# Performance work log

Measured on AMD Instinct MI355X. Metric: run time of the kernel, lower is better.

Reference implementation:

```python
import jax, jax.numpy as jnp
import numpy as np
from jax import lax

DIM = 512
HEADS = 8
SR = 2  # kernel_and_stride for the KV downsampling conv


def setup_inputs() -> dict:
    key = jax.random.key(0)
    k0, k1, k2, k3 = jax.random.split(key, 4)
    B, C, H, W = 4, DIM, 64, 64
    x = jax.random.normal(k0, (B, C, H, W), dtype=jnp.float32)
    # Conv weights in OIHW layout (matching torch)
    wq = jax.random.normal(k1, (C, C, 1, 1), dtype=jnp.float32) / np.sqrt(C)
    wkv = jax.random.normal(k2, (2 * C, C, SR, SR), dtype=jnp.float32) / np.sqrt(C * SR * SR)
    wout = jax.random.normal(k3, (C, C, 1, 1), dtype=jnp.float32) / np.sqrt(C)
    return {"x": x, "wq": wq, "wkv": wkv, "wout": wout}


def _attend(x, wq, wkv, wout):
    B, C, H, W = x.shape
    d = C // HEADS
    scale = d ** -0.5
    # to_q: 1x1 conv == channel matmul
    q = jnp.einsum('bchw,oc->bohw', x, wq[:, :, 0, 0])
    # to_kv: strided conv, downsamples spatial grid by SR
    kv = lax.conv_general_dilated(
        x, wkv, window_strides=(SR, SR), padding='VALID',
        dimension_numbers=('NCHW', 'OIHW', 'NCHW'))
    k, v = jnp.split(kv, 2, axis=1)  # each [B, C, H/SR, W/SR]

    def to_bhl(t):  # [B, (h d), X, Y] -> [B, h, X*Y, d]
        b, c, xh, xw = t.shape
        return t.reshape(b, HEADS, d, xh * xw).transpose(0, 1, 3, 2)

    qh, kh, vh = to_bhl(q), to_bhl(k), to_bhl(v)
    sim = jnp.einsum('bhid,bhjd->bhij', qh, kh) * scale
    attn = jax.nn.softmax(sim, axis=-1)
    out = jnp.einsum('bhij,bhjd->bhid', attn, vh)  # [B, h, HW, d]
    out = out.transpose(0, 1, 3, 2).reshape(B, C, H, W)
    return jnp.einsum('bchw,oc->bohw', out, wout[:, :, 0, 0])


def reference(x, wq, wkv, wout):
    return _attend(x, wq, wkv, wout)
```

## Files before the change

### kernel.cpp

```cpp
#include <hip/hip_runtime.h>
#include <hip/hip_bf16.h>

typedef __bf16 bf16x8 __attribute__((ext_vector_type(8)));
typedef float f32x4 __attribute__((ext_vector_type(4)));
typedef unsigned short ushort_t;
typedef ushort_t ushort8 __attribute__((ext_vector_type(8)));
typedef unsigned uint2v __attribute__((ext_vector_type(2)));
typedef unsigned uint4v __attribute__((ext_vector_type(4)));

#define DIM 512
#define HEADS 8
#define HD 64
#define HWN 4096
#define KVN 1024
#define KKV 2048
#define LOG2E 1.44269504f

__device__ __forceinline__ ushort_t f2bf(float f) {
    union { float f; unsigned u; } v; v.f = f;
    unsigned r = v.u + 0x7fffu + ((v.u >> 16) & 1u);
    return (ushort_t)(r >> 16);
}

__device__ __forceinline__ unsigned cvtpk(float lo, float hi) {
    unsigned r;
    asm("v_cvt_pk_bf16_f32 %0, %1, %2" : "=v"(r) : "v"(lo), "v"(hi));
    return r;
}

__device__ __forceinline__ void pl32swap(unsigned &a, unsigned &b) {
    asm("v_permlane32_swap_b32 %0, %1" : "+v"(a), "+v"(b));
}
__device__ __forceinline__ void pl16swap(unsigned &a, unsigned &b) {
    asm("v_permlane16_swap_b32 %0, %1" : "+v"(a), "+v"(b));
}

__device__ __forceinline__ bf16x8 frag4(unsigned a, unsigned b, unsigned c, unsigned d) {
    uint4v t; t[0] = a; t[1] = b; t[2] = c; t[3] = d;
    return __builtin_bit_cast(bf16x8, t);
}

__device__ __forceinline__ void gload_lds16(const ushort_t* g, ushort_t* l) {
    __builtin_amdgcn_global_load_lds(
        (const __attribute__((address_space(1))) unsigned int*)(const void*)g,
        (__attribute__((address_space(3))) unsigned int*)(void*)l,
        16, 0, 0);
}

__device__ __forceinline__ void drain_sync() {
    asm volatile("s_waitcnt vmcnt(0)" ::: "memory");
    __syncthreads();
}

__global__ __launch_bounds__(256) void cvt_w2_kernel(
        const float* __restrict__ wq, const float* __restrict__ wout,
        ushort_t* __restrict__ wqb, ushort_t* __restrict__ woutb) {
    int i = blockIdx.x * 256 + threadIdx.x;
    const float* src;
    ushort_t* dst;
    if (i < 32768) { src = &wq[(size_t)i * 8];              dst = &wqb[(size_t)i * 8]; }
    else           { src = &wout[(size_t)(i - 32768) * 8];  dst = &woutb[(size_t)(i - 32768) * 8]; }
    f32x4 v0 = *(const f32x4*)&src[0];
    f32x4 v1 = *(const f32x4*)&src[4];
    ushort8 w;
    w[0] = f2bf(v0[0]); w[1] = f2bf(v0[1]); w[2] = f2bf(v0[2]); w[3] = f2bf(v0[3]);
    w[4] = f2bf(v1[0]); w[5] = f2bf(v1[1]); w[6] = f2bf(v1[2]); w[7] = f2bf(v1[3]);
    *(ushort8*)dst = w;
}

__global__ __launch_bounds__(256) void cvt_xT_kernel(
        const float* __restrict__ x, ushort_t* __restrict__ xT) {
    const int b  = blockIdx.z;
    const int c0 = blockIdx.y * 64;
    const int p0 = blockIdx.x * 64;
    __shared__ ushort_t tile[64 * 72];

    const int tid = threadIdx.x;
    {
        int r = tid >> 2, pc = (tid & 3) * 16;
        const float* src = &x[((size_t)b * DIM + c0 + r) * HWN + p0 + pc];
        f32x4 v0 = *(const f32x4*)&src[0];
        f32x4 v1 = *(const f32x4*)&src[4];
        f32x4 v2 = *(const f32x4*)&src[8];
        f32x4 v3 = *(const f32x4*)&src[12];
        ushort8 w0, w1;
        w0[0]=f2bf(v0[0]); w0[1]=f2bf(v0[1]); w0[2]=f2bf(v0[2]); w0[3]=f2bf(v0[3]);
        w0[4]=f2bf(v1[0]); w0[5]=f2bf(v1[1]); w0[6]=f2bf(v1[2]); w0[7]=f2bf(v1[3]);
        w1[0]=f2bf(v2[0]); w1[1]=f2bf(v2[1]); w1[2]=f2bf(v2[2]); w1[3]=f2bf(v2[3]);
        w1[4]=f2bf(v3[0]); w1[5]=f2bf(v3[1]); w1[6]=f2bf(v3[2]); w1[7]=f2bf(v3[3]);
        *(ushort8*)&tile[r * 72 + pc]     = w0;
        *(ushort8*)&tile[r * 72 + pc + 8] = w1;
    }
    __syncthreads();
    {
        int p = tid >> 2, cc = (tid & 3) * 16;
        ushort8 w0, w1;
        #pragma unroll
        for (int j = 0; j < 8; ++j) {
            w0[j] = tile[(cc + j) * 72 + p];
            w1[j] = tile[(cc + 8 + j) * 72 + p];
        }
        ushort_t* dst = &xT[((size_t)b * HWN + p0 + p) * DIM + c0 + cc];
        *(ushort8*)&dst[0] = w0;
        *(ushort8*)&dst[8] = w1;
    }
}

__global__ __launch_bounds__(256) void cvt_wkvT_kernel(
        const float* __restrict__ wkv, ushort_t* __restrict__ wkvT) {
    int i = blockIdx.x * 256 + threadIdx.x;
    if (i >= 1024 * 512) return;
    int o2 = i >> 9, c = i & 511;
    f32x4 v = *(const f32x4*)&wkv[(size_t)i * 4];
    #pragma unroll
    for (int q = 0; q < 4; ++q)
        wkvT[(size_t)o2 * KKV + q * 512 + c] = f2bf(v[q]);
}

__device__ __forceinline__ void gemm_compute_512(
        const ushort_t* __restrict__ sA, const ushort_t* __restrict__ sB,
        int wm, int wn, int l15, int quad, f32x4 (&acc)[4][2]) {
    bf16x8 a[2][4], bb[2][2];
    #pragma unroll
    for (int kk = 0; kk < 2; ++kk) {
        #pragma unroll
        for (int i = 0; i < 4; ++i) {
            int ra = wm + i * 16 + l15;
            a[kk][i] = *(const bf16x8*)&sA[ra * 64 + (((kk * 4 + quad) ^ (ra & 7)) * 8)];
        }
        #pragma unroll
        for (int j = 0; j < 2; ++j) {
            int rb = wn + j * 16 + l15;
            bb[kk][j] = *(const bf16x8*)&sB[rb * 64 + (((kk * 4 + quad) ^ (rb & 7)) * 8)];
        }
    }
    #pragma unroll
    for (int i = 0; i < 4; ++i)
        #pragma unroll
        for (int j = 0; j < 2; ++j) {
            acc[i][j] = __builtin_amdgcn_mfma_f32_16x16x32_bf16(a[0][i], bb[0][j], acc[i][j], 0, 0, 0);
            acc[i][j] = __builtin_amdgcn_mfma_f32_16x16x32_bf16(a[1][i], bb[1][j], acc[i][j], 0, 0, 0);
        }
}

__global__ __launch_bounds__(512, 4) void qproj_kernel(
        const ushort_t* __restrict__ xT, const ushort_t* __restrict__ wqb,
        ushort_t* __restrict__ qs) {
    const int b  = blockIdx.z;
    const int m0 = blockIdx.y * 128;
    const int n0 = blockIdx.x * 128;

    __shared__ ushort_t shA[2][128 * 64];
    __shared__ ushort_t shB[2][128 * 64];

    const int tid  = threadIdx.x;
    const int wave = tid >> 6;
    const int lane = tid & 63;
    const int l15  = lane & 15;
    const int quad = lane >> 4;
    const int wm   = (wave >> 2) * 64;
    const int wn   = (wave & 3) * 32;
    const int r8   = lane >> 3;
    const int c8   = (lane & 7) ^ r8;

    const ushort_t* aS[2];
    const ushort_t* bS[2];
    #pragma unroll
    for (int g = 0; g < 2; ++g) {
        int row = g * 64 + wave * 8 + r8;
        aS[g] = &wqb[(size_t)(m0 + row) * DIM + c8 * 8];
        bS[g] = &xT[((size_t)b * HWN + n0 + row) * DIM + c8 * 8];
    }
    const int ldso = wave * 8 * 64;

    f32x4 zero = {0.f, 0.f, 0.f, 0.f};
    f32x4 acc[4][2];
    #pragma unroll
    for (int i = 0; i < 4; ++i)
        #pragma unroll
        for (int j = 0; j < 2; ++j) acc[i][j] = zero;

    #pragma unroll
    for (int g = 0; g < 2; ++g) {
        gload_lds16(aS[g], &shA[0][g * 4096 + ldso]);
        gload_lds16(bS[g], &shB[0][g * 4096 + ldso]);
    }
    drain_sync();

    for (int t = 0; t < 8; ++t) {
        const int cur = t & 1;
        if (t < 7) {
            const int ko = (t + 1) * 64;
            #pragma unroll
            for (int g = 0; g < 2; ++g) {
                gload_lds16(aS[g] + ko, &shA[cur ^ 1][g * 4096 + ldso]);
                gload_lds16(bS[g] + ko, &shB[cur ^ 1][g * 4096 + ldso]);
            }
        }
        gemm_compute_512(shA[cur], shB[cur], wm, wn, l15, quad, acc);
        drain_sync();
    }

    #pragma unroll
    for (int i = 0; i < 4; ++i)
        #pragma unroll
        for (int j = 0; j < 2; ++j)
            #pragma unroll
            for (int r = 0; r < 4; ++r) {
                int m = m0 + wm + i * 16 + quad * 4 + r;
                int n = n0 + wn + j * 16 + l15;
                qs[((size_t)b * DIM + m) * HWN + n] =
                    f2bf(acc[i][j][r] * (0.125f * LOG2E));
            }
}

__global__ __launch_bounds__(512, 4) void kv_kernel(
        const ushort_t* __restrict__ xT, const ushort_t* __restrict__ wkvT,
        ushort_t* __restrict__ ks, ushort_t* __restrict__ vt) {
    const int b  = blockIdx.z;
    const int m0 = blockIdx.y * 64;
    const int j0 = blockIdx.x * 128;

    __shared__ ushort_t shA[2][64 * 64];
    __shared__ ushort_t shB[2][128 * 64];

    const int tid  = threadIdx.x;
    const int wave = tid >> 6;
    const int lane = tid & 63;
    const int l15  = lane & 15;
    const int quad = lane >> 4;
    const int wm   = (wave >> 2) * 32;
    const int wn   = (wave & 3) * 32;
    const int r8   = lane >> 3;
    const int c8   = (lane & 7) ^ r8;

    const ushort_t* aS = &wkvT[(size_t)(m0 + wave * 8 + r8) * KKV + c8 * 8];
    const ushort_t* bS[2];
    #pragma unroll
    for (int g = 0; g < 2; ++g) {
        int row = g * 64 + wave * 8 + r8;
        int jr = j0 + row;
        int y = jr >> 5, x = jr & 31;
        bS[g] = &xT[((size_t)b * HWN + 128 * y + 2 * x) * DIM + c8 * 8];
    }
    const int ldso = wave * 8 * 64;

    f32x4 zero = {0.f, 0.f, 0.f, 0.f};
    f32x4 acc[2][2];
    #pragma unroll
    for (int i = 0; i < 2; ++i)
        #pragma unroll
        for (int j = 0; j < 2; ++j) acc[i][j] = zero;

    gload_lds16(aS, &shA[0][ldso]);
    #pragma unroll
    for (int g = 0; g < 2; ++g)
        gload_lds16(bS[g], &shB[0][g * 4096 + ldso]);
    drain_sync();

    for (int t = 0; t < 32; ++t) {
        const int cur = t & 1;
        if (t < 31) {
            const int tn = t + 1;
            const int qn = tn >> 3;
            const int ao = tn * 64;
            const int bo = (64 * (qn >> 1) + (qn & 1)) * DIM + (tn & 7) * 64;
            gload_lds16(aS + ao, &shA[cur ^ 1][ldso]);
            #pragma unroll
            for (int g = 0; g < 2; ++g)
                gload_lds16(bS[g] + bo, &shB[cur ^ 1][g * 4096 + ldso]);
        }
        {
            bf16x8 a[2][2], bb[2][2];
            #pragma unroll
            for (int kk = 0; kk < 2; ++kk) {
                #pragma unroll
                for (int i = 0; i < 2; ++i) {
                    int ra = wm + i * 16 + l15;
                    a[kk][i] = *(const bf16x8*)&shA[cur][ra * 64 + (((kk * 4 + quad) ^ (ra & 7)) * 8)];
                }
                #pragma unroll
                for (int j = 0; j < 2; ++j) {
                    int rb = wn + j * 16 + l15;
                    bb[kk][j] = *(const bf16x8*)&shB[cur][rb * 64 + (((kk * 4 + quad) ^ (rb & 7)) * 8)];
                }
            }
            #pragma unroll
            for (int i = 0; i < 2; ++i)
                #pragma unroll
                for (int j = 0; j < 2; ++j) {
                    acc[i][j] = __builtin_amdgcn_mfma_f32_16x16x32_bf16(a[0][i], bb[0][j], acc[i][j], 0, 0, 0);
                    acc[i][j] = __builtin_amdgcn_mfma_f32_16x16x32_bf16(a[1][i], bb[1][j], acc[i][j], 0, 0, 0);
                }
        }
        drain_sync();
    }

    if (m0 < DIM) {
        const int h = m0 >> 6;
        ushort_t* cbuf = &shB[0][0];
        #pragma unroll
        for (int i = 0; i < 2; ++i)
            #pragma unroll
            for (int j = 0; j < 2; ++j)
                #pragma unroll
                for (int r = 0; r < 4; ++r) {
                    int m = wm + i * 16 + quad * 4 + r;
                    int n = wn + j * 16 + l15;
                    cbuf[n * 72 + m] = f2bf(acc[i][j][r]);
                }
        __syncthreads();
        {
            int n = tid >> 2, doff = (tid & 3) * 16;
            ushort8 u0 = *(const ushort8*)&cbuf[n * 72 + doff];
            ushort8 u1 = *(const ushort8*)&cbuf[n * 72 + doff + 8];
            ushort_t* dst =
                &ks[(((size_t)b * HEADS + h) * KVN + j0 + n) * HD + doff];
            *(ushort8*)&dst[0] = u0;
            *(ushort8*)&dst[8] = u1;
        }
    } else {
        const int h = (m0 - DIM) >> 6;
        #pragma unroll
        for (int i = 0; i < 2; ++i)
            #pragma unroll
            for (int j = 0; j < 2; ++j)
                #pragma unroll
                for (int r = 0; r < 4; ++r) {
                    int dd = wm + i * 16 + quad * 4 + r;
                    int n  = wn + j * 16 + l15;
                    vt[(((size_t)b * HEADS + h) * HD + dd) * KVN + j0 + n] =
                        f2bf(acc[i][j][r]);
                }
    }
}

__global__ __launch_bounds__(256, 2) void attn_kernel(
        const ushort_t* __restrict__ qs,
        const ushort_t* __restrict__ ks,
        const ushort_t* __restrict__ vt,
        ushort_t* __restrict__ ao) {
    const int b = blockIdx.z, h = blockIdx.y;
    const int tid = threadIdx.x, wave = tid >> 6, lane = tid & 63;
    const int l15 = lane & 15, quad = lane >> 4;
    const int s7  = l15 & 7;
    const int iw = blockIdx.x * 256 + wave * 64;

    __shared__ ushort_t ldsK[2][64 * 64];
    __shared__ ushort_t ldsV[2][64 * 64];

    const ushort_t* Kh = &ks[((size_t)b * HEADS + h) * (KVN * HD)];
    const ushort_t* Vh = &vt[((size_t)b * HEADS + h) * (HD * KVN)];

    const int srow = wave * 8 + (lane >> 3);
    const int schk = (lane & 7) ^ (lane >> 3);
    const ushort_t* kp0 = Kh + srow * HD + schk * 8;
    const ushort_t* kp1 = Kh + (srow + 32) * HD + schk * 8;
    const ushort_t* vp0 = Vh + (size_t)srow * KVN + schk * 8;
    const ushort_t* vp1 = Vh + (size_t)(srow + 32) * KVN + schk * 8;

    bf16x8 bq[4][2];
    #pragma unroll
    for (int ih = 0; ih < 4; ++ih)
        #pragma unroll
        for (int kk = 0; kk < 2; ++kk) {
            ushort8 t;
            #pragma unroll
            for (int j = 0; j < 8; ++j) {
                int c = h * HD + kk * 32 + quad * 8 + j;
                int p = iw + ih * 16 + l15;
                t[j] = qs[((size_t)b * DIM + c) * HWN + p];
            }
            bq[ih][kk] = *(bf16x8*)&t;
        }

    f32x4 zero = {0.f, 0.f, 0.f, 0.f};
    f32x4 o[4][4];
    #pragma unroll
    for (int ih = 0; ih < 4; ++ih)
        #pragma unroll
        for (int nt = 0; nt < 4; ++nt) o[ih][nt] = zero;
    float ssum[4] = {0.f, 0.f, 0.f, 0.f};

    gload_lds16(kp0, &ldsK[0][wave * 512]);
    gload_lds16(kp1, &ldsK[0][wave * 512 + 2048]);
    gload_lds16(vp0, &ldsV[0][wave * 512]);
    gload_lds16(vp1, &ldsV[0][wave * 512 + 2048]);
    asm volatile("s_waitcnt vmcnt(0)" ::: "memory");
    __syncthreads();

    for (int t = 0; t < 16; ++t) {
        const int cur = t & 1;
        if (t < 15) {
            const int jn = (t + 1) * 64;
            gload_lds16(kp0 + jn * HD, &ldsK[cur ^ 1][wave * 512]);
            gload_lds16(kp1 + jn * HD, &ldsK[cur ^ 1][wave * 512 + 2048]);
            gload_lds16(vp0 + jn,      &ldsV[cur ^ 1][wave * 512]);
            gload_lds16(vp1 + jn,      &ldsV[cur ^ 1][wave * 512 + 2048]);
        }

        unsigned P2[4][4][2];
        #pragma unroll
        for (int nt = 0; nt < 4; ++nt) {
            const ushort_t* kb = &ldsK[cur][(nt * 16 + l15) * 64];
            bf16x8 bk0 = *(const bf16x8*)&kb[(quad ^ s7) * 8];
            bf16x8 bk1 = *(const bf16x8*)&kb[((quad + 4) ^ s7) * 8];
            #pragma unroll
            for (int ih = 0; ih < 4; ++ih) {
                f32x4 s = zero;
                s = __builtin_amdgcn_mfma_f32_16x16x32_bf16(bk0, bq[ih][0], s, 0, 0, 0);
                s = __builtin_amdgcn_mfma_f32_16x16x32_bf16(bk1, bq[ih][1], s, 0, 0, 0);
                float p0 = __builtin_amdgcn_exp2f(s[0]);
                float p1 = __builtin_amdgcn_exp2f(s[1]);
                float p2 = __builtin_amdgcn_exp2f(s[2]);
                float p3 = __builtin_amdgcn_exp2f(s[3]);
                ssum[ih] += (p0 + p1) + (p2 + p3);
                P2[ih][nt][0] = cvtpk(p0, p1);
                P2[ih][nt][1] = cvtpk(p2, p3);
            }
        }

        #pragma unroll
        for (int ih = 0; ih < 4; ++ih)
            #pragma unroll
            for (int bh = 0; bh < 2; ++bh)
                #pragma unroll
                for (int rp = 0; rp < 2; ++rp) {
                    pl32swap(P2[ih][bh * 2][rp], P2[ih][bh * 2 + 1][rp]);
                    pl16swap(P2[ih][bh * 2][rp], P2[ih][bh * 2 + 1][rp]);
                }
        bf16x8 bp[4][2];
        #pragma unroll
        for (int ih = 0; ih < 4; ++ih) {
            bp[ih][0] = frag4(P2[ih][0][0], P2[ih][0][1], P2[ih][1][0], P2[ih][1][1]);
            bp[ih][1] = frag4(P2[ih][2][0], P2[ih][2][1], P2[ih][3][0], P2[ih][3][1]);
        }

        #pragma unroll
        for (int nt = 0; nt < 4; ++nt) {
            const ushort_t* vb = &ldsV[cur][(nt * 16 + l15) * 64];
            bf16x8 bv0 = *(const bf16x8*)&vb[(quad ^ s7) * 8];
            bf16x8 bv1 = *(const bf16x8*)&vb[((quad + 4) ^ s7) * 8];
            #pragma unroll
            for (int ih = 0; ih < 4; ++ih) {
                o[ih][nt] = __builtin_amdgcn_mfma_f32_16x16x32_bf16(bv0, bp[ih][0], o[ih][nt], 0, 0, 0);
                o[ih][nt] = __builtin_amdgcn_mfma_f32_16x16x32_bf16(bv1, bp[ih][1], o[ih][nt], 0, 0, 0);
            }
        }

        asm volatile("s_waitcnt vmcnt(0)" ::: "memory");
        __syncthreads();
    }

    #pragma unroll
    for (int ih = 0; ih < 4; ++ih) {
        float tsum = ssum[ih];
        tsum += __shfl_xor(tsum, 16);
        tsum += __shfl_xor(tsum, 32);
        float invl = 1.0f / tsum;
        int i = iw + ih * 16 + l15;
        ushort_t* dst = &ao[((size_t)b * HWN + i) * DIM + h * HD];
        #pragma unroll
        for (int nt = 0; nt < 4; ++nt) {
            unsigned d0 = cvtpk(o[ih][nt][0] * invl, o[ih][nt][1] * invl);
            unsigned d1 = cvtpk(o[ih][nt][2] * invl, o[ih][nt][3] * invl);
            uint2v w; w[0] = d0; w[1] = d1;
            *(uint2v*)&dst[nt * 16 + quad * 4] = w;
        }
    }
}

__global__ __launch_bounds__(512, 4) void outproj_kernel(
        const ushort_t* __restrict__ ao, const ushort_t* __restrict__ woutb,
        float* __restrict__ out) {
    const int b  = blockIdx.z;
    const int m0 = blockIdx.y * 128;
    const int n0 = blockIdx.x * 128;

    __shared__ ushort_t shA[2][128 * 64];
    __shared__ ushort_t shB[2][128 * 64];

    const int tid  = threadIdx.x;
    const int wave = tid >> 6;
    const int lane = tid & 63;
    const int l15  = lane & 15;
    const int quad = lane >> 4;
    const int wm   = (wave >> 2) * 64;
    const int wn   = (wave & 3) * 32;
    const int r8   = lane >> 3;
    const int c8   = (lane & 7) ^ r8;

    const ushort_t* aS[2];
    const ushort_t* bS[2];
    #pragma unroll
    for (int g = 0; g < 2; ++g) {
        int row = g * 64 + wave * 8 + r8;
        aS[g] = &woutb[(size_t)(m0 + row) * DIM + c8 * 8];
        bS[g] = &ao[((size_t)b * HWN + n0 + row) * DIM + c8 * 8];
    }
    const int ldso = wave * 8 * 64;

    f32x4 zero = {0.f, 0.f, 0.f, 0.f};
    f32x4 acc[4][2];
    #pragma unroll
    for (int i = 0; i < 4; ++i)
        #pragma unroll
        for (int j = 0; j < 2; ++j) acc[i][j] = zero;

    #pragma unroll
    for (int g = 0; g < 2; ++g) {
        gload_lds16(aS[g], &shA[0][g * 4096 + ldso]);
        gload_lds16(bS[g], &shB[0][g * 4096 + ldso]);
    }
    drain_sync();

    for (int t = 0; t < 8; ++t) {
        const int cur = t & 1;
        if (t < 7) {
            const int ko = (t + 1) * 64;
            #pragma unroll
            for (int g = 0; g < 2; ++g) {
                gload_lds16(aS[g] + ko, &shA[cur ^ 1][g * 4096 + ldso]);
                gload_lds16(bS[g] + ko, &shB[cur ^ 1][g * 4096 + ldso]);
            }
        }
        gemm_compute_512(shA[cur], shB[cur], wm, wn, l15, quad, acc);
        drain_sync();
    }

    #pragma unroll
    for (int i = 0; i < 4; ++i)
        #pragma unroll
        for (int j = 0; j < 2; ++j)
            #pragma unroll
            for (int r = 0; r < 4; ++r) {
                int m = m0 + wm + i * 16 + quad * 4 + r;
                int n = n0 + wn + j * 16 + l15;
                out[((size_t)b * DIM + m) * HWN + n] = acc[i][j][r];
            }
}

extern "C" void kernel_launch(void* const* d_in, const int* in_sizes, int n_in,
                              void* d_out, int out_size, void* d_ws, size_t ws_size,
                              hipStream_t stream) {
    const float* x    = (const float*)d_in[0];
    const float* wq   = (const float*)d_in[1];
    const float* wkv  = (const float*)d_in[2];
    const float* wout = (const float*)d_in[3];
    float* out = (float*)d_out;

    char* ws = (char*)d_ws;
    ushort_t* xT    = (ushort_t*)(ws);
    ushort_t* qsb   = (ushort_t*)(ws + 16777216);
    ushort_t* ksb   = (ushort_t*)(ws + 33554432);
    ushort_t* vtb   = (ushort_t*)(ws + 37748736);
    ushort_t* aob   = (ushort_t*)(ws + 41943040);
    ushort_t* wqb   = (ushort_t*)(ws + 58720256);
    ushort_t* wkvT  = (ushort_t*)(ws + 59244544);
    ushort_t* woutb = (ushort_t*)(ws + 63438848);

    cvt_xT_kernel  <<<dim3(64, 8, 4), 256, 0, stream>>>(x, xT);
    cvt_w2_kernel  <<<dim3(256),      256, 0, stream>>>(wq, wout, wqb, woutb);
    cvt_wkvT_kernel<<<dim3(2048),     256, 0, stream>>>(wkv, wkvT);

    qproj_kernel  <<<dim3(32, 4, 4),  512, 0, stream>>>(xT, wqb, qsb);
    kv_kernel     <<<dim3(8, 16, 4),  512, 0, stream>>>(xT, wkvT, ksb, vtb);
    attn_kernel   <<<dim3(16, 8, 4),  256, 0, stream>>>(qsb, ksb, vtb, aob);
    outproj_kernel<<<dim3(32, 4, 4),  512, 0, stream>>>(aob, woutb, out);
}
```

Measured before the change: 192.0 us.

## Triple-buffer LDS pipelines in projection GEMM kernels with partial vmcnt waits

Converts the double-buffered global-to-LDS pipelines in the q-projection, kv and output-projection kernels into three-stage pipelines that prefetch two K-tiles ahead. Each iteration now waits with a partial vmcnt instead of draining all loads, keeping one tile in flight during compute. This raises LDS use per block (96 KB for the 128x128 kernels), and launch_bounds no longer requests 4 blocks per CU, so occupancy may fall.

New measurement: 201.2 us. 1.05x slower.

```diff
diff --git a/kernel.cpp b/kernel.cpp
--- a/kernel.cpp
+++ b/kernel.cpp
@@ -143,15 +143,15 @@
         }
 }
 
-__global__ __launch_bounds__(512, 4) void qproj_kernel(
+__global__ __launch_bounds__(512) void qproj_kernel(
         const ushort_t* __restrict__ xT, const ushort_t* __restrict__ wqb,
         ushort_t* __restrict__ qs) {
     const int b  = blockIdx.z;
     const int m0 = blockIdx.y * 128;
     const int n0 = blockIdx.x * 128;
 
-    __shared__ ushort_t shA[2][128 * 64];
-    __shared__ ushort_t shB[2][128 * 64];
+    __shared__ ushort_t shA[3][128 * 64];
+    __shared__ ushort_t shB[3][128 * 64];
 
     const int tid  = threadIdx.x;
     const int wave = tid >> 6;
@@ -181,25 +181,32 @@
         for (int j = 0; j < 2; ++j) acc[i][j] = zero;
 
     #pragma unroll
-    for (int g = 0; g < 2; ++g) {
-        gload_lds16(aS[g], &shA[0][g * 4096 + ldso]);
-        gload_lds16(bS[g], &shB[0][g * 4096 + ldso]);
-    }
-    drain_sync();
-
-    for (int t = 0; t < 8; ++t) {
-        const int cur = t & 1;
-        if (t < 7) {
-            const int ko = (t + 1) * 64;
+    for (int s = 0; s < 2; ++s)
+        #pragma unroll
+        for (int g = 0; g < 2; ++g) {
+            gload_lds16(aS[g] + s * 64, &shA[s][g * 4096 + ldso]);
+            gload_lds16(bS[g] + s * 64, &shB[s][g * 4096 + ldso]);
+        }
+
+    int cur = 0;
+    for (int t = 0; t < 7; ++t) {
+        asm volatile("s_waitcnt vmcnt(4)" ::: "memory");
+        __syncthreads();
+        if (t < 6) {
+            const int ko = (t + 2) * 64;
+            int c2 = cur + 2; if (c2 >= 3) c2 -= 3;
             #pragma unroll
             for (int g = 0; g < 2; ++g) {
-                gload_lds16(aS[g] + ko, &shA[cur ^ 1][g * 4096 + ldso]);
-                gload_lds16(bS[g] + ko, &shB[cur ^ 1][g * 4096 + ldso]);
+                gload_lds16(aS[g] + ko, &shA[c2][g * 4096 + ldso]);
+                gload_lds16(bS[g] + ko, &shB[c2][g * 4096 + ldso]);
             }
         }
         gemm_compute_512(shA[cur], shB[cur], wm, wn, l15, quad, acc);
-        drain_sync();
-    }
+        cur = (cur == 2) ? 0 : cur + 1;
+    }
+    asm volatile("s_waitcnt vmcnt(0)" ::: "memory");
+    __syncthreads();
+    gemm_compute_512(shA[cur], shB[cur], wm, wn, l15, quad, acc);
 
     #pragma unroll
     for (int i = 0; i < 4; ++i)
@@ -214,15 +221,15 @@
             }
 }
 
-__global__ __launch_bounds__(512, 4) void kv_kernel(
+__global__ __launch_bounds__(512) void kv_kernel(
         const ushort_t* __restrict__ xT, const ushort_t* __restrict__ wkvT,
         ushort_t* __restrict__ ks, ushort_t* __restrict__ vt) {
     const int b  = blockIdx.z;
     const int m0 = blockIdx.y * 64;
     const int j0 = blockIdx.x * 128;
 
-    __shared__ ushort_t shA[2][64 * 64];
-    __shared__ ushort_t shB[2][128 * 64];
+    __shared__ ushort_t shA[3][64 * 64];
+    __shared__ ushort_t shB[3][128 * 64];
 
     const int tid  = threadIdx.x;
     const int wave = tid >> 6;
@@ -252,23 +259,28 @@
         #pragma unroll
         for (int j = 0; j < 2; ++j) acc[i][j] = zero;
 
-    gload_lds16(aS, &shA[0][ldso]);
-    #pragma unroll
-    for (int g = 0; g < 2; ++g)
-        gload_lds16(bS[g], &shB[0][g * 4096 + ldso]);
-    drain_sync();
-
-    for (int t = 0; t < 32; ++t) {
-        const int cur = t & 1;
-        if (t < 31) {
-            const int tn = t + 1;
+    #pragma unroll
+    for (int s = 0; s < 2; ++s) {
+        gload_lds16(aS + s * 64, &shA[s][ldso]);
+        #pragma unroll
+        for (int g = 0; g < 2; ++g)
+            gload_lds16(bS[g] + s * 64, &shB[s][g * 4096 + ldso]);
+    }
+
+    int cur = 0;
+    for (int t = 0; t < 31; ++t) {
+        asm volatile("s_waitcnt vmcnt(3)" ::: "memory");
+        __syncthreads();
+        if (t < 30) {
+            const int tn = t + 2;
             const int qn = tn >> 3;
             const int ao = tn * 64;
             const int bo = (64 * (qn >> 1) + (qn & 1)) * DIM + (tn & 7) * 64;
-            gload_lds16(aS + ao, &shA[cur ^ 1][ldso]);
+            int c2 = cur + 2; if (c2 >= 3) c2 -= 3;
+            gload_lds16(aS + ao, &shA[c2][ldso]);
             #pragma unroll
             for (int g = 0; g < 2; ++g)
-                gload_lds16(bS[g] + bo, &shB[cur ^ 1][g * 4096 + ldso]);
+                gload_lds16(bS[g] + bo, &shB[c2][g * 4096 + ldso]);
         }
         {
             bf16x8 a[2][2], bb[2][2];
@@ -293,10 +305,36 @@
                     acc[i][j] = __builtin_amdgcn_mfma_f32_16x16x32_bf16(a[1][i], bb[1][j], acc[i][j], 0, 0, 0);
                 }
         }
-        drain_sync();
+        cur = (cur == 2) ? 0 : cur + 1;
+    }
+    asm volatile("s_waitcnt vmcnt(0)" ::: "memory");
+    __syncthreads();
+    {
+        bf16x8 a[2][2], bb[2][2];
+        #pragma unroll
+        for (int kk = 0; kk < 2; ++kk) {
+            #pragma unroll
+            for (int i = 0; i < 2; ++i) {
+                int ra = wm + i * 16 + l15;
+                a[kk][i] = *(const bf16x8*)&shA[cur][ra * 64 + (((kk * 4 + quad) ^ (ra & 7)) * 8)];
+            }
+            #pragma unroll
+            for (int j = 0; j < 2; ++j) {
+                int rb = wn + j * 16 + l15;
+                bb[kk][j] = *(const bf16x8*)&shB[cur][rb * 64 + (((kk * 4 + quad) ^ (rb & 7)) * 8)];
+            }
+        }
+        #pragma unroll
+        for (int i = 0; i < 2; ++i)
+            #pragma unroll
+            for (int j = 0; j < 2; ++j) {
+                acc[i][j] = __builtin_amdgcn_mfma_f32_16x16x32_bf16(a[0][i], bb[0][j], acc[i][j], 0, 0, 0);
+                acc[i][j] = __builtin_amdgcn_mfma_f32_16x16x32_bf16(a[1][i], bb[1][j], acc[i][j], 0, 0, 0);
+            }
     }
 
     if (m0 < DIM) {
+        __syncthreads();
         const int h = m0 >> 6;
         ushort_t* cbuf = &shB[0][0];
         #pragma unroll
@@ -470,15 +508,15 @@
     }
 }
 
-__global__ __launch_bounds__(512, 4) void outproj_kernel(
+__global__ __launch_bounds__(512) void outproj_kernel(
         const ushort_t* __restrict__ ao, const ushort_t* __restrict__ woutb,
         float* __restrict__ out) {
     const int b  = blockIdx.z;
     const int m0 = blockIdx.y * 128;
     const int n0 = blockIdx.x * 128;
 
-    __shared__ ushort_t shA[2][128 * 64];
-    __shared__ ushort_t shB[2][128 * 64];
+    __shared__ ushort_t shA[3][128 * 64];
+    __shared__ ushort_t shB[3][128 * 64];
 
     const int tid  = threadIdx.x;
     const int wave = tid >> 6;
@@ -508,25 +546,32 @@
         for (int j = 0; j < 2; ++j) acc[i][j] = zero;
 
     #pragma unroll
-    for (int g = 0; g < 2; ++g) {
-        gload_lds16(aS[g], &shA[0][g * 4096 + ldso]);
-        gload_lds16(bS[g], &shB[0][g * 4096 + ldso]);
-    }
-    drain_sync();
-
-    for (int t = 0; t < 8; ++t) {
-        const int cur = t & 1;
-        if (t < 7) {
-            const int ko = (t + 1) * 64;
+    for (int s = 0; s < 2; ++s)
+        #pragma unroll
+        for (int g = 0; g < 2; ++g) {
+            gload_lds16(aS[g] + s * 64, &shA[s][g * 4096 + ldso]);
+            gload_lds16(bS[g] + s * 64, &shB[s][g * 4096 + ldso]);
+        }
+
+    int cur = 0;
+    for (int t = 0; t < 7; ++t) {
+        asm volatile("s_waitcnt vmcnt(4)" ::: "memory");
+        __syncthreads();
+        if (t < 6) {
+            const int ko = (t + 2) * 64;
+            int c2 = cur + 2; if (c2 >= 3) c2 -= 3;
             #pragma unroll
             for (int g = 0; g < 2; ++g) {
-                gload_lds16(aS[g] + ko, &shA[cur ^ 1][g * 4096 + ldso]);
-                gload_lds16(bS[g] + ko, &shB[cur ^ 1][g * 4096 + ldso]);
+                gload_lds16(aS[g] + ko, &shA[c2][g * 4096 + ldso]);
+                gload_lds16(bS[g] + ko, &shB[c2][g * 4096 + ldso]);
             }
         }
         gemm_compute_512(shA[cur], shB[cur], wm, wn, l15, quad, acc);
-        drain_sync();
-    }
+        cur = (cur == 2) ? 0 : cur + 1;
+    }
+    asm volatile("s_waitcnt vmcnt(0)" ::: "memory");
+    __syncthreads();
+    gemm_compute_512(shA[cur], shB[cur], wm, wn, l15, quad, acc);
 
     #pragma unroll
     for (int i = 0; i < 4; ++i)
```
